# Performance work log

Measured on AMD Instinct MI355X. Metric: run time of the kernel, lower is better.

The kernel has to match this reference:

```python
import jax, jax.numpy as jnp
import numpy as np

INV_SQRT_2 = 0.5 ** 0.5


def setup_inputs() -> dict:
    key = jax.random.key(0)
    k1, k2, k3, k4, k5 = jax.random.split(key, 5)
    B, N, E, D_IN, D_OUT = 2, 50000, 800000, 64, 64
    x = jax.random.normal(k1, (B, N, D_IN), dtype=jnp.float32)
    src = jax.random.randint(k2, (E,), 0, N, dtype=jnp.int64)
    dst = jax.random.randint(k3, (E,), 0, N, dtype=jnp.int64)
    # nn.Linear weights: (dim_out, dim_in), bias=False
    W_src = jax.random.normal(k4, (D_OUT, D_IN), dtype=jnp.float32) / np.sqrt(D_IN)
    W_dst = jax.random.normal(k5, (D_OUT, D_IN), dtype=jnp.float32) / np.sqrt(D_IN)
    return {"x": x, "src": src, "dst": dst, "W_src": W_src, "W_dst": W_dst}


def reference(x, src, dst, W_src, W_dst):
    # Equivalent math to linear(x[:, src]) + linear(x[:, dst]):
    # transform each node once, then gather per edge (avoids redundant GEMM work).
    hs = jnp.einsum('bnd,ed->bne', x, W_src)  # (B, N, D_out)
    hd = jnp.einsum('bnd,ed->bne', x, W_dst)  # (B, N, D_out)
    return (hs[:, src] + hd[:, dst]) * INV_SQRT_2  # (B, E, D_out)
```

## Files before the change

### kernel.cpp

```cpp
#include <hip/hip_runtime.h>

#define INV_SQRT2 0.70710678118654752440f

typedef __attribute__((ext_vector_type(8))) short bf16x8;
typedef __attribute__((ext_vector_type(4))) float f32x4;

__device__ __forceinline__ unsigned short f32_to_bf16_rne(float f) {
    unsigned int u = __builtin_bit_cast(unsigned int, f);
    u += 0x7FFFu + ((u >> 16) & 1u);
    return (unsigned short)(u >> 16);
}
__device__ __forceinline__ float bf16_to_f32(unsigned short h) {
    return __builtin_bit_cast(float, ((unsigned int)h) << 16);
}

__global__ __launch_bounds__(256) void convert_k(
    const float* __restrict__ x,
    const float* __restrict__ Wsrc,
    const float* __restrict__ Wdst,
    unsigned short* __restrict__ xb,
    unsigned short* __restrict__ Wb,
    long long nx, int nw)
{
    long long t = (long long)blockIdx.x * 256 + threadIdx.x;
    long long total8 = (nx + 2LL * nw) >> 3;
    if (t >= total8) return;
    long long base = t << 3;

    const float* sp;
    unsigned short* dp;
    if (base < nx)            { sp = x    + base;            dp = xb + base; }
    else if (base < nx + nw)  { sp = Wsrc + (base - nx);      dp = Wb + (base - nx); }
    else                      { sp = Wdst + (base - nx - nw); dp = Wb + (base - nx); }

    float4 a = ((const float4*)sp)[0];
    float4 b = ((const float4*)sp)[1];
    uint4 o;
    o.x = (unsigned)f32_to_bf16_rne(a.x) | ((unsigned)f32_to_bf16_rne(a.y) << 16);
    o.y = (unsigned)f32_to_bf16_rne(a.z) | ((unsigned)f32_to_bf16_rne(a.w) << 16);
    o.z = (unsigned)f32_to_bf16_rne(b.x) | ((unsigned)f32_to_bf16_rne(b.y) << 16);
    o.w = (unsigned)f32_to_bf16_rne(b.z) | ((unsigned)f32_to_bf16_rne(b.w) << 16);
    *((uint4*)dp) = o;
}

__global__ __launch_bounds__(256) void transform_mfma_k(
    const unsigned short* __restrict__ xb,
    const unsigned short* __restrict__ Wb,
    unsigned short* __restrict__ hb,
    int rows)
{
    int wave = (blockIdx.x * 256 + threadIdx.x) >> 6;
    int lane = threadIdx.x & 63;
    int row_tiles = (rows + 15) >> 4;
    if (wave >= row_tiles) return;

    int m    = lane & 15;
    int quad = lane >> 4;

    int arow_i = wave * 16 + m;
    if (arow_i >= rows) arow_i = rows - 1;
    const bf16x8* arow = (const bf16x8*)(xb + (size_t)arow_i * 64);
    bf16x8 a0 = arow[quad];
    bf16x8 a1 = arow[4 + quad];

    f32x4 acc[8];
#pragma unroll
    for (int ct = 0; ct < 8; ++ct) {
        int n = ct * 16 + m;
        const bf16x8* brow = (const bf16x8*)(Wb + (size_t)n * 64);
        bf16x8 b0 = brow[quad];
        bf16x8 b1 = brow[4 + quad];
        f32x4 c = {0.f, 0.f, 0.f, 0.f};
        c = __builtin_amdgcn_mfma_f32_16x16x32_bf16(a0, b0, c, 0, 0, 0);
        c = __builtin_amdgcn_mfma_f32_16x16x32_bf16(a1, b1, c, 0, 0, 0);
        acc[ct] = c;
    }

#pragma unroll
    for (int ct = 0; ct < 8; ++ct) {
#pragma unroll
        for (int r = 0; r < 4; ++r) {
            int orow = wave * 16 + quad * 4 + r;
            if (orow < rows) {
                hb[(size_t)orow * 128 + ct * 16 + m] =
                    f32_to_bf16_rne(acc[ct][r] * INV_SQRT2);
            }
        }
    }
}

__global__ __launch_bounds__(256) void gather_k(
    const unsigned short* __restrict__ hb,
    const int* __restrict__ src,
    const int* __restrict__ dst,
    float4* __restrict__ out,
    int E, int N)
{
    int t = blockIdx.x * 256 + threadIdx.x;
    if (t >= E * 16) return;
    int e = t >> 4;
    int c = t & 15;
    int b = blockIdx.y;

    int s = src[e];
    int d = dst[e];

    const unsigned short* ps = hb + ((size_t)(b * N + s)) * 128 + c * 4;
    const unsigned short* pd = hb + ((size_t)(b * N + d)) * 128 + 64 + c * 4;
    ushort4 us = *(const ushort4*)ps;
    ushort4 ud = *(const ushort4*)pd;

    float4 o;
    o.x = bf16_to_f32(us.x) + bf16_to_f32(ud.x);
    o.y = bf16_to_f32(us.y) + bf16_to_f32(ud.y);
    o.z = bf16_to_f32(us.z) + bf16_to_f32(ud.z);
    o.w = bf16_to_f32(us.w) + bf16_to_f32(ud.w);

    out[((size_t)b * E + e) * 16 + c] = o;
}

__global__ __launch_bounds__(256) void fused_fallback_k(
    const float* __restrict__ x,
    const int* __restrict__ src,
    const int* __restrict__ dst,
    const float* __restrict__ Wsrc,
    const float* __restrict__ Wdst,
    float* __restrict__ out,
    int E, int N)
{
    int t = blockIdx.x * 256 + threadIdx.x;
    if (t >= E * 64) return;
    int o = t & 63;
    int e = t >> 6;
    int b = blockIdx.y;

    const float* xs = x + ((size_t)(b * N + src[e])) * 64;
    const float* xd = x + ((size_t)(b * N + dst[e])) * 64;
    const float* ws = Wsrc + o * 64;
    const float* wd = Wdst + o * 64;
    float acc = 0.0f;
#pragma unroll
    for (int k = 0; k < 64; ++k) {
        acc = fmaf(xs[k], ws[k], acc);
        acc = fmaf(xd[k], wd[k], acc);
    }
    out[((size_t)b * E + e) * 64 + o] = acc * INV_SQRT2;
}

extern "C" void kernel_launch(void* const* d_in, const int* in_sizes, int n_in,
                              void* d_out, int out_size, void* d_ws, size_t ws_size,
                              hipStream_t stream)
{
    const float* x    = (const float*)d_in[0];
    const int*   src  = (const int*)d_in[1];
    const int*   dst  = (const int*)d_in[2];
    const float* Wsrc = (const float*)d_in[3];
    const float* Wdst = (const float*)d_in[4];
    float* out = (float*)d_out;

    const int E = in_sizes[1];
    const long long xsz = in_sizes[0];
    const int B = (int)((long long)out_size / ((long long)E * 64));
    const int N = (int)(xsz / ((long long)B * 64));
    const int rows = B * N;

    const size_t xb_elems = (size_t)rows * 64;
    const size_t wb_elems = 128 * 64;
    const size_t hb_elems = (size_t)rows * 128;
    const size_t need = (xb_elems + wb_elems + hb_elems) * sizeof(unsigned short);

    if (ws_size >= need) {
        unsigned short* xb = (unsigned short*)d_ws;
        unsigned short* Wb = xb + xb_elems;
        unsigned short* hb = Wb + wb_elems;

        long long nx = (long long)rows * 64;
        int nw = 64 * 64;
        long long total8 = (nx + 2LL * nw) >> 3;
        int g0 = (int)((total8 + 255) / 256);
        convert_k<<<g0, 256, 0, stream>>>(x, Wsrc, Wdst, xb, Wb, nx, nw);

        int row_tiles = (rows + 15) >> 4;
        int g1 = (row_tiles + 3) / 4;
        transform_mfma_k<<<g1, 256, 0, stream>>>(xb, Wb, hb, rows);

        dim3 g2((E * 16 + 255) / 256, B);
        gather_k<<<g2, 256, 0, stream>>>(hb, src, dst, (float4*)out, E, N);
    } else {
        dim3 g((E * 64 + 255) / 256, B);
        fused_fallback_k<<<g, 256, 0, stream>>>(x, src, dst, Wsrc, Wdst, out, E, N);
    }
}
```

Measured before the change: 505.2 us.

## Widen gather to 16-byte loads, handle both batches per thread, nontemporal stores

The gather kernel now has each thread handle 8 bf16 channels for both batch entries. It issues 16-byte vector loads and writes outputs with nontemporal stores. This is meant to cut thread and index-load overhead, reuse the src/dst index reads across batches, and keep the large streaming output from polluting cache. The fast path is now hardcoded to B==2, and other batch sizes fall back to the slow fused kernel.

```diff
diff --git a/kernel.cpp b/kernel.cpp
--- a/kernel.cpp
+++ b/kernel.cpp
@@ -4,6 +4,7 @@
 
 typedef __attribute__((ext_vector_type(8))) short bf16x8;
 typedef __attribute__((ext_vector_type(4))) float f32x4;
+typedef __attribute__((ext_vector_type(8))) unsigned short u16x8;
 
 __device__ __forceinline__ unsigned short f32_to_bf16_rne(float f) {
     unsigned int u = __builtin_bit_cast(unsigned int, f);
@@ -93,30 +94,49 @@
     const unsigned short* __restrict__ hb,
     const int* __restrict__ src,
     const int* __restrict__ dst,
-    float4* __restrict__ out,
+    f32x4* __restrict__ out,
     int E, int N)
 {
     int t = blockIdx.x * 256 + threadIdx.x;
-    if (t >= E * 16) return;
-    int e = t >> 4;
-    int c = t & 15;
-    int b = blockIdx.y;
+    if (t >= E * 8) return;
+    int e = t >> 3;
+    int c = t & 7;
 
     int s = src[e];
     int d = dst[e];
 
-    const unsigned short* ps = hb + ((size_t)(b * N + s)) * 128 + c * 4;
-    const unsigned short* pd = hb + ((size_t)(b * N + d)) * 128 + 64 + c * 4;
-    ushort4 us = *(const ushort4*)ps;
-    ushort4 ud = *(const ushort4*)pd;
-
-    float4 o;
-    o.x = bf16_to_f32(us.x) + bf16_to_f32(ud.x);
-    o.y = bf16_to_f32(us.y) + bf16_to_f32(ud.y);
-    o.z = bf16_to_f32(us.z) + bf16_to_f32(ud.z);
-    o.w = bf16_to_f32(us.w) + bf16_to_f32(ud.w);
-
-    out[((size_t)b * E + e) * 16 + c] = o;
+    const unsigned short* h0 = hb;
+    const unsigned short* h1 = hb + (size_t)N * 128;
+
+    u16x8 us0 = *(const u16x8*)(h0 + (size_t)s * 128 + c * 8);
+    u16x8 ud0 = *(const u16x8*)(h0 + (size_t)d * 128 + 64 + c * 8);
+    u16x8 us1 = *(const u16x8*)(h1 + (size_t)s * 128 + c * 8);
+    u16x8 ud1 = *(const u16x8*)(h1 + (size_t)d * 128 + 64 + c * 8);
+
+    f32x4 o0a, o0b, o1a, o1b;
+    o0a[0] = bf16_to_f32(us0[0]) + bf16_to_f32(ud0[0]);
+    o0a[1] = bf16_to_f32(us0[1]) + bf16_to_f32(ud0[1]);
+    o0a[2] = bf16_to_f32(us0[2]) + bf16_to_f32(ud0[2]);
+    o0a[3] = bf16_to_f32(us0[3]) + bf16_to_f32(ud0[3]);
+    o0b[0] = bf16_to_f32(us0[4]) + bf16_to_f32(ud0[4]);
+    o0b[1] = bf16_to_f32(us0[5]) + bf16_to_f32(ud0[5]);
+    o0b[2] = bf16_to_f32(us0[6]) + bf16_to_f32(ud0[6]);
+    o0b[3] = bf16_to_f32(us0[7]) + bf16_to_f32(ud0[7]);
+    o1a[0] = bf16_to_f32(us1[0]) + bf16_to_f32(ud1[0]);
+    o1a[1] = bf16_to_f32(us1[1]) + bf16_to_f32(ud1[1]);
+    o1a[2] = bf16_to_f32(us1[2]) + bf16_to_f32(ud1[2]);
+    o1a[3] = bf16_to_f32(us1[3]) + bf16_to_f32(ud1[3]);
+    o1b[0] = bf16_to_f32(us1[4]) + bf16_to_f32(ud1[4]);
+    o1b[1] = bf16_to_f32(us1[5]) + bf16_to_f32(ud1[5]);
+    o1b[2] = bf16_to_f32(us1[6]) + bf16_to_f32(ud1[6]);
+    o1b[3] = bf16_to_f32(us1[7]) + bf16_to_f32(ud1[7]);
+
+    size_t o0 = (size_t)e * 16 + (size_t)(c * 2);
+    __builtin_nontemporal_store(o0a, &out[o0]);
+    __builtin_nontemporal_store(o0b, &out[o0 + 1]);
+    size_t o1 = ((size_t)E + (size_t)e) * 16 + (size_t)(c * 2);
+    __builtin_nontemporal_store(o1a, &out[o1]);
+    __builtin_nontemporal_store(o1b, &out[o1 + 1]);
 }
 
 __global__ __launch_bounds__(256) void fused_fallback_k(
@@ -169,7 +189,7 @@
     const size_t hb_elems = (size_t)rows * 128;
     const size_t need = (xb_elems + wb_elems + hb_elems) * sizeof(unsigned short);
 
-    if (ws_size >= need) {
+    if (ws_size >= need && B == 2) {
         unsigned short* xb = (unsigned short*)d_ws;
         unsigned short* Wb = xb + xb_elems;
         unsigned short* hb = Wb + wb_elems;
@@ -184,8 +204,8 @@
         int g1 = (row_tiles + 3) / 4;
         transform_mfma_k<<<g1, 256, 0, stream>>>(xb, Wb, hb, rows);
 
-        dim3 g2((E * 16 + 255) / 256, B);
-        gather_k<<<g2, 256, 0, stream>>>(hb, src, dst, (float4*)out, E, N);
+        int g2 = (E * 8 + 255) / 256;
+        gather_k<<<g2, 256, 0, stream>>>(hb, src, dst, (f32x4*)out, E, N);
     } else {
         dim3 g((E * 64 + 255) / 256, B);
         fused_fallback_k<<<g, 256, 0, stream>>>(x, src, dst, Wsrc, Wdst, out, E, N);
```

New measurement: 499.8 us. Within noise of the previous version (-1.1%).

## Fuse x bf16 conversion into MFMA transform and widen gather with nontemporal stores

Applied to the files above, without the earlier changes.

Drops the separate pass that converts x to bf16; the transform kernel now reads fp32 x directly and converts in registers, which removes a full write and re-read of x. Only the weights are still converted, by a tiny kernel. The gather kernel now has each thread handle two edges and both batches, loading src/dst indices once as int2. It uses 16-byte loads and nontemporal 16-byte stores for the large output. The fast path is restricted to B==2 and even E, otherwise the fused fallback runs.

```diff
diff --git a/kernel.cpp b/kernel.cpp
--- a/kernel.cpp
+++ b/kernel.cpp
@@ -4,6 +4,7 @@
 
 typedef __attribute__((ext_vector_type(8))) short bf16x8;
 typedef __attribute__((ext_vector_type(4))) float f32x4;
+typedef __attribute__((ext_vector_type(8))) unsigned short u16x8;
 
 __device__ __forceinline__ unsigned short f32_to_bf16_rne(float f) {
     unsigned int u = __builtin_bit_cast(unsigned int, f);
@@ -14,24 +15,17 @@
     return __builtin_bit_cast(float, ((unsigned int)h) << 16);
 }
 
-__global__ __launch_bounds__(256) void convert_k(
-    const float* __restrict__ x,
+__global__ __launch_bounds__(256) void convert_w_k(
     const float* __restrict__ Wsrc,
     const float* __restrict__ Wdst,
-    unsigned short* __restrict__ xb,
-    unsigned short* __restrict__ Wb,
-    long long nx, int nw)
-{
-    long long t = (long long)blockIdx.x * 256 + threadIdx.x;
-    long long total8 = (nx + 2LL * nw) >> 3;
-    if (t >= total8) return;
-    long long base = t << 3;
-
-    const float* sp;
-    unsigned short* dp;
-    if (base < nx)            { sp = x    + base;            dp = xb + base; }
-    else if (base < nx + nw)  { sp = Wsrc + (base - nx);      dp = Wb + (base - nx); }
-    else                      { sp = Wdst + (base - nx - nw); dp = Wb + (base - nx); }
+    unsigned short* __restrict__ Wb)
+{
+    int t = blockIdx.x * 256 + threadIdx.x;
+    if (t >= 1024) return;
+    int base = t * 8;
+
+    const float* sp = (base < 4096) ? (Wsrc + base) : (Wdst + (base - 4096));
+    unsigned short* dp = Wb + base;
 
     float4 a = ((const float4*)sp)[0];
     float4 b = ((const float4*)sp)[1];
@@ -44,7 +38,7 @@
 }
 
 __global__ __launch_bounds__(256) void transform_mfma_k(
-    const unsigned short* __restrict__ xb,
+    const float* __restrict__ x,
     const unsigned short* __restrict__ Wb,
     unsigned short* __restrict__ hb,
     int rows)
@@ -59,9 +53,29 @@
 
     int arow_i = wave * 16 + m;
     if (arow_i >= rows) arow_i = rows - 1;
-    const bf16x8* arow = (const bf16x8*)(xb + (size_t)arow_i * 64);
-    bf16x8 a0 = arow[quad];
-    bf16x8 a1 = arow[4 + quad];
+    const float4* arow = (const float4*)(x + (size_t)arow_i * 64);
+    float4 f0 = arow[quad * 2];
+    float4 f1 = arow[quad * 2 + 1];
+    float4 f2 = arow[8 + quad * 2];
+    float4 f3 = arow[8 + quad * 2 + 1];
+
+    bf16x8 a0, a1;
+    a0[0] = (short)f32_to_bf16_rne(f0.x);
+    a0[1] = (short)f32_to_bf16_rne(f0.y);
+    a0[2] = (short)f32_to_bf16_rne(f0.z);
+    a0[3] = (short)f32_to_bf16_rne(f0.w);
+    a0[4] = (short)f32_to_bf16_rne(f1.x);
+    a0[5] = (short)f32_to_bf16_rne(f1.y);
+    a0[6] = (short)f32_to_bf16_rne(f1.z);
+    a0[7] = (short)f32_to_bf16_rne(f1.w);
+    a1[0] = (short)f32_to_bf16_rne(f2.x);
+    a1[1] = (short)f32_to_bf16_rne(f2.y);
+    a1[2] = (short)f32_to_bf16_rne(f2.z);
+    a1[3] = (short)f32_to_bf16_rne(f2.w);
+    a1[4] = (short)f32_to_bf16_rne(f3.x);
+    a1[5] = (short)f32_to_bf16_rne(f3.y);
+    a1[6] = (short)f32_to_bf16_rne(f3.z);
+    a1[7] = (short)f32_to_bf16_rne(f3.w);
 
     f32x4 acc[8];
 #pragma unroll
@@ -89,34 +103,56 @@
     }
 }
 
+__device__ __forceinline__ void sum_store(const u16x8 a, const u16x8 b,
+                                          f32x4* __restrict__ out, size_t o4)
+{
+    f32x4 lo, hi;
+    lo[0] = bf16_to_f32(a[0]) + bf16_to_f32(b[0]);
+    lo[1] = bf16_to_f32(a[1]) + bf16_to_f32(b[1]);
+    lo[2] = bf16_to_f32(a[2]) + bf16_to_f32(b[2]);
+    lo[3] = bf16_to_f32(a[3]) + bf16_to_f32(b[3]);
+    hi[0] = bf16_to_f32(a[4]) + bf16_to_f32(b[4]);
+    hi[1] = bf16_to_f32(a[5]) + bf16_to_f32(b[5]);
+    hi[2] = bf16_to_f32(a[6]) + bf16_to_f32(b[6]);
+    hi[3] = bf16_to_f32(a[7]) + bf16_to_f32(b[7]);
+    __builtin_nontemporal_store(lo, &out[o4]);
+    __builtin_nontemporal_store(hi, &out[o4 + 1]);
+}
+
 __global__ __launch_bounds__(256) void gather_k(
     const unsigned short* __restrict__ hb,
     const int* __restrict__ src,
     const int* __restrict__ dst,
-    float4* __restrict__ out,
+    f32x4* __restrict__ out,
     int E, int N)
 {
     int t = blockIdx.x * 256 + threadIdx.x;
-    if (t >= E * 16) return;
-    int e = t >> 4;
-    int c = t & 15;
-    int b = blockIdx.y;
-
-    int s = src[e];
-    int d = dst[e];
-
-    const unsigned short* ps = hb + ((size_t)(b * N + s)) * 128 + c * 4;
-    const unsigned short* pd = hb + ((size_t)(b * N + d)) * 128 + 64 + c * 4;
-    ushort4 us = *(const ushort4*)ps;
-    ushort4 ud = *(const ushort4*)pd;
-
-    float4 o;
-    o.x = bf16_to_f32(us.x) + bf16_to_f32(ud.x);
-    o.y = bf16_to_f32(us.y) + bf16_to_f32(ud.y);
-    o.z = bf16_to_f32(us.z) + bf16_to_f32(ud.z);
-    o.w = bf16_to_f32(us.w) + bf16_to_f32(ud.w);
-
-    out[((size_t)b * E + e) * 16 + c] = o;
+    if (t >= E * 4) return;
+    int p = t >> 3;
+    int c = t & 7;
+    int e0 = p * 2;
+
+    int2 sp = *(const int2*)(src + e0);
+    int2 dp = *(const int2*)(dst + e0);
+
+    const unsigned short* h0 = hb;
+    const unsigned short* h1 = hb + (size_t)N * 128;
+    const int off = c * 8;
+
+    u16x8 us0a = *(const u16x8*)(h0 + (size_t)sp.x * 128 + off);
+    u16x8 ud0a = *(const u16x8*)(h0 + (size_t)dp.x * 128 + 64 + off);
+    u16x8 us1a = *(const u16x8*)(h1 + (size_t)sp.x * 128 + off);
+    u16x8 ud1a = *(const u16x8*)(h1 + (size_t)dp.x * 128 + 64 + off);
+    u16x8 us0b = *(const u16x8*)(h0 + (size_t)sp.y * 128 + off);
+    u16x8 ud0b = *(const u16x8*)(h0 + (size_t)dp.y * 128 + 64 + off);
+    u16x8 us1b = *(const u16x8*)(h1 + (size_t)sp.y * 128 + off);
+    u16x8 ud1b = *(const u16x8*)(h1 + (size_t)dp.y * 128 + 64 + off);
+
+    size_t c2 = (size_t)(c * 2);
+    sum_store(us0a, ud0a, out, (size_t)e0 * 16 + c2);
+    sum_store(us1a, ud1a, out, ((size_t)E + e0) * 16 + c2);
+    sum_store(us0b, ud0b, out, (size_t)(e0 + 1) * 16 + c2);
+    sum_store(us1b, ud1b, out, ((size_t)E + e0 + 1) * 16 + c2);
 }
 
 __global__ __launch_bounds__(256) void fused_fallback_k(
@@ -164,28 +200,22 @@
     const int N = (int)(xsz / ((long long)B * 64));
     const int rows = B * N;
 
-    const size_t xb_elems = (size_t)rows * 64;
     const size_t wb_elems = 128 * 64;
     const size_t hb_elems = (size_t)rows * 128;
-    const size_t need = (xb_elems + wb_elems + hb_elems) * sizeof(unsigned short);
-
-    if (ws_size >= need) {
-        unsigned short* xb = (unsigned short*)d_ws;
-        unsigned short* Wb = xb + xb_elems;
+    const size_t need = (wb_elems + hb_elems) * sizeof(unsigned short);
+
+    if (ws_size >= need && B == 2 && (E & 1) == 0) {
+        unsigned short* Wb = (unsigned short*)d_ws;
         unsigned short* hb = Wb + wb_elems;
 
-        long long nx = (long long)rows * 64;
-        int nw = 64 * 64;
-        long long total8 = (nx + 2LL * nw) >> 3;
-        int g0 = (int)((total8 + 255) / 256);
-        convert_k<<<g0, 256, 0, stream>>>(x, Wsrc, Wdst, xb, Wb, nx, nw);
+        convert_w_k<<<4, 256, 0, stream>>>(Wsrc, Wdst, Wb);
 
         int row_tiles = (rows + 15) >> 4;
         int g1 = (row_tiles + 3) / 4;
-        transform_mfma_k<<<g1, 256, 0, stream>>>(xb, Wb, hb, rows);
-
-        dim3 g2((E * 16 + 255) / 256, B);
-        gather_k<<<g2, 256, 0, stream>>>(hb, src, dst, (float4*)out, E, N);
+        transform_mfma_k<<<g1, 256, 0, stream>>>(x, Wb, hb, rows);
+
+        int g2 = (E * 4 + 255) / 256;
+        gather_k<<<g2, 256, 0, stream>>>(hb, src, dst, (f32x4*)out, E, N);
     } else {
         dim3 g((E * 64 + 255) / 256, B);
         fused_fallback_k<<<g, 256, 0, stream>>>(x, src, dst, Wsrc, Wdst, out, E, N);
```

After: 505.9 us. About the same (+0.1%).
